# Kernel optimization log

Measured on AMD Instinct MI355X. Metric: run time of the kernel, lower is better.

## Reference

```python
import jax, jax.numpy as jnp
import numpy as np

B, C, N = 16, 256, 64
L = N * N
RED = 16  # SE reduction
ANGLES = (0, 90, 180, 270)
R = len(ANGLES)


def _d2xy(n, d):
    """Classic Hilbert curve distance -> (x, y) on an n x n grid (n power of 2)."""
    x = y = 0
    t = d
    s = 1
    while s < n:
        rx = 1 & (t // 2)
        ry = 1 & (t ^ rx)
        if ry == 0:
            if rx == 1:
                x = s - 1 - x
                y = s - 1 - y
            x, y = y, x
        x += s * rx
        y += s * ry
        t //= 4
        s *= 2
    return x, y


def _make_rot_idx(n, angles):
    coords = []
    for d in range(n * n):
        x, y = _d2xy(n, d)
        coords.append((y, x))  # original stores (row, col) = (y, x)
    idx_map = {coord: i for i, coord in enumerate(coords)}
    all_inv = []
    for angle in angles:
        inv = []
        for r, c in coords:
            if angle == 0:
                r0, c0 = r, c
            elif angle == 90:
                r0, c0 = c, n - 1 - r
            elif angle == 180:
                r0, c0 = n - 1 - r, n - 1 - c
            else:
                r0, c0 = n - 1 - c, r
            inv.append(idx_map[(r0, c0)])
        all_inv.append(inv)
    return np.asarray(all_inv, dtype=np.int32)  # [R, L]


def setup_inputs() -> dict:
    key = jax.random.key(0)
    k1, k2, k3 = jax.random.split(key, 3)
    x = jax.random.normal(k1, (B, C, L), dtype=jnp.float32)
    rot_idx = jnp.asarray(_make_rot_idx(N, ANGLES))  # [R, L] int32
    w1 = jax.random.normal(k2, (C, RED), dtype=jnp.float32) * (1.0 / np.sqrt(C))
    b1 = jnp.zeros((RED,), dtype=jnp.float32)
    w2 = jax.random.normal(k3, (RED, C), dtype=jnp.float32) * (1.0 / np.sqrt(RED))
    b2 = jnp.zeros((C,), dtype=jnp.float32)
    return {"x": x, "rot_idx": rot_idx, "w1": w1, "b1": b1, "w2": w2, "b2": b2}


def reference(x, rot_idx, w1, b1, w2, b2):
    # Gather the 4 Hilbert-order rotation permutations: [B, C, R, L]
    x_rot = x[:, :, rot_idx]
    # RotationChannelAttention (SE over channels, softmax over rotations)
    s = jnp.mean(x_rot, axis=3)                                   # [B, C, R]
    h = jax.nn.relu(jnp.einsum('bcr,ck->bkr', s, w1) + b1[None, :, None])
    scores = jnp.einsum('bkr,kc->bcr', h, w2) + b2[None, :, None]  # [B, C, R]
    w = jax.nn.softmax(scores, axis=2)                             # over rotations
    x_f = jnp.einsum('bcr,bcrl->bcl', w, x_rot)                    # [B, C, L]
    return x_f
```

## Files before the change

### kernel.cpp

```cpp
#include <hip/hip_runtime.h>


constexpr int Lconst = 4096;
constexpr int BC     = 16 * 256;

__global__ __launch_bounds__(256) void rotavg_kernel(
    const float* __restrict__ x,
    const int*   __restrict__ rot_idx,
    float*       __restrict__ out) {
  __shared__ float row[Lconst];

  const int bc = blockIdx.x;
  const float* xr = x + (size_t)bc * Lconst;
  float*       o  = out + (size_t)bc * Lconst;
  const int t = threadIdx.x;

  const float4* xr4  = reinterpret_cast<const float4*>(xr);
  float4*       row4 = reinterpret_cast<float4*>(row);
#pragma unroll
  for (int i = 0; i < 4; ++i) {
    row4[t + i * 256] = xr4[t + i * 256];
  }
  __syncthreads();

  const int4* idx0 = reinterpret_cast<const int4*>(rot_idx);
  const int4* idx1 = reinterpret_cast<const int4*>(rot_idx + Lconst);
  const int4* idx2 = reinterpret_cast<const int4*>(rot_idx + 2 * Lconst);
  const int4* idx3 = reinterpret_cast<const int4*>(rot_idx + 3 * Lconst);
  float4* o4 = reinterpret_cast<float4*>(o);

#pragma unroll
  for (int i = 0; i < 4; ++i) {
    const int e = t + i * 256;
    const int4 a = idx0[e];
    const int4 b = idx1[e];
    const int4 c = idx2[e];
    const int4 d = idx3[e];
    float4 v;
    v.x = 0.25f * (row[a.x] + row[b.x] + row[c.x] + row[d.x]);
    v.y = 0.25f * (row[a.y] + row[b.y] + row[c.y] + row[d.y]);
    v.z = 0.25f * (row[a.z] + row[b.z] + row[c.z] + row[d.z]);
    v.w = 0.25f * (row[a.w] + row[b.w] + row[c.w] + row[d.w]);
    o4[e] = v;
  }
}

extern "C" void kernel_launch(void* const* d_in, const int* in_sizes, int n_in,
                              void* d_out, int out_size, void* d_ws, size_t ws_size,
                              hipStream_t stream) {
  const float* x       = (const float*)d_in[0];
  const int*   rot_idx = (const int*)d_in[1];
  float* out = (float*)d_out;

  rotavg_kernel<<<BC, 256, 0, stream>>>(x, rot_idx, out);
}
```

Baseline: 28.81 us.

## Pack rotation indices into per-quad metadata and gather float4 quads from LDS

A small prep kernel compresses the three non-identity rotation index tables into one uint2 per 4-element group. Each entry holds a base quad index per rotation plus 2-bit lane selectors. The main kernel then does three float4 LDS reads per output quad instead of sixteen scalar reads, and one uint2 global load instead of four int4 loads. The identity rotation is taken from registers. This relies on rotation 0 being the identity and on each aligned quad mapping to a single aligned quad under rotation, which holds for the Hilbert layout. It also adds a second kernel launch and a workspace write.

```diff
diff --git a/kernel.cpp b/kernel.cpp
--- a/kernel.cpp
+++ b/kernel.cpp
@@ -1,46 +1,69 @@
 #include <hip/hip_runtime.h>
 
 
-constexpr int Lconst = 4096;
-constexpr int BC     = 16 * 256;
+constexpr int Lq  = 4096;
+constexpr int NQ  = Lq / 4;
+constexpr int BC  = 16 * 256;
+
+__global__ __launch_bounds__(256) void prep_kernel(
+    const int* __restrict__ rot, uint2* __restrict__ meta) {
+  const int q = blockIdx.x * 256 + threadIdx.x;
+  const int4* r90  = reinterpret_cast<const int4*>(rot + Lq);
+  const int4* r180 = reinterpret_cast<const int4*>(rot + 2 * Lq);
+  const int4* r270 = reinterpret_cast<const int4*>(rot + 3 * Lq);
+  const int4 a = r90[q], b = r180[q], c = r270[q];
+  const uint b90  = (uint)a.x >> 2;
+  const uint b180 = (uint)b.x >> 2;
+  const uint b270 = (uint)c.x >> 2;
+  const uint p90  = (uint)(a.x & 3) | ((uint)(a.y & 3) << 2) |
+                    ((uint)(a.z & 3) << 4) | ((uint)(a.w & 3) << 6);
+  const uint p180 = (uint)(b.x & 3) | ((uint)(b.y & 3) << 2) |
+                    ((uint)(b.z & 3) << 4) | ((uint)(b.w & 3) << 6);
+  const uint p270 = (uint)(c.x & 3) | ((uint)(c.y & 3) << 2) |
+                    ((uint)(c.z & 3) << 4) | ((uint)(c.w & 3) << 6);
+  meta[q] = make_uint2(b90 | (b180 << 10) | (b270 << 20),
+                       p90 | (p180 << 8) | (p270 << 16));
+}
+
+__device__ __forceinline__ float sel(const float4 q, const uint c) {
+  return c == 0u ? q.x : (c == 1u ? q.y : (c == 2u ? q.z : q.w));
+}
 
 __global__ __launch_bounds__(256) void rotavg_kernel(
     const float* __restrict__ x,
-    const int*   __restrict__ rot_idx,
+    const uint2* __restrict__ meta,
     float*       __restrict__ out) {
-  __shared__ float row[Lconst];
+  __shared__ float4 row4[NQ];
 
   const int bc = blockIdx.x;
-  const float* xr = x + (size_t)bc * Lconst;
-  float*       o  = out + (size_t)bc * Lconst;
+  const float4* xr4 = reinterpret_cast<const float4*>(x + (size_t)bc * Lq);
+  float4*       o4  = reinterpret_cast<float4*>(out + (size_t)bc * Lq);
   const int t = threadIdx.x;
 
-  const float4* xr4  = reinterpret_cast<const float4*>(xr);
-  float4*       row4 = reinterpret_cast<float4*>(row);
+  float4 xq[4];
+  uint2  mm[4];
 #pragma unroll
   for (int i = 0; i < 4; ++i) {
-    row4[t + i * 256] = xr4[t + i * 256];
+    const int e = t + i * 256;
+    xq[i] = xr4[e];
+    row4[e] = xq[i];
+    mm[i] = meta[e];
   }
   __syncthreads();
-
-  const int4* idx0 = reinterpret_cast<const int4*>(rot_idx);
-  const int4* idx1 = reinterpret_cast<const int4*>(rot_idx + Lconst);
-  const int4* idx2 = reinterpret_cast<const int4*>(rot_idx + 2 * Lconst);
-  const int4* idx3 = reinterpret_cast<const int4*>(rot_idx + 3 * Lconst);
-  float4* o4 = reinterpret_cast<float4*>(o);
 
 #pragma unroll
   for (int i = 0; i < 4; ++i) {
     const int e = t + i * 256;
-    const int4 a = idx0[e];
-    const int4 b = idx1[e];
-    const int4 c = idx2[e];
-    const int4 d = idx3[e];
+    const uint2 m = mm[i];
+    const float4 q90  = row4[m.x & 1023u];
+    const float4 q180 = row4[(m.x >> 10) & 1023u];
+    const float4 q270 = row4[(m.x >> 20) & 1023u];
+    const uint p = m.y;
     float4 v;
-    v.x = 0.25f * (row[a.x] + row[b.x] + row[c.x] + row[d.x]);
-    v.y = 0.25f * (row[a.y] + row[b.y] + row[c.y] + row[d.y]);
-    v.z = 0.25f * (row[a.z] + row[b.z] + row[c.z] + row[d.z]);
-    v.w = 0.25f * (row[a.w] + row[b.w] + row[c.w] + row[d.w]);
+    v.x = 0.25f * (xq[i].x + sel(q90, p & 3u)         + sel(q180, (p >> 8) & 3u)  + sel(q270, (p >> 16) & 3u));
+    v.y = 0.25f * (xq[i].y + sel(q90, (p >> 2) & 3u)  + sel(q180, (p >> 10) & 3u) + sel(q270, (p >> 18) & 3u));
+    v.z = 0.25f * (xq[i].z + sel(q90, (p >> 4) & 3u)  + sel(q180, (p >> 12) & 3u) + sel(q270, (p >> 20) & 3u));
+    v.w = 0.25f * (xq[i].w + sel(q90, (p >> 6) & 3u)  + sel(q180, (p >> 14) & 3u) + sel(q270, (p >> 22) & 3u));
     o4[e] = v;
   }
 }
@@ -51,6 +74,8 @@
   const float* x       = (const float*)d_in[0];
   const int*   rot_idx = (const int*)d_in[1];
   float* out = (float*)d_out;
+  uint2* meta = (uint2*)d_ws;
 
-  rotavg_kernel<<<BC, 256, 0, stream>>>(x, rot_idx, out);
+  prep_kernel<<<NQ / 256, 256, 0, stream>>>(rot_idx, meta);
+  rotavg_kernel<<<BC, 256, 0, stream>>>(x, meta, out);
 }
```

Result: slower. 33.80 us (+17.3%).

## Process four rows per block with register-cached packed indices and double-buffered LDS

Applied to the files above, without the earlier changes.

Each block now handles four (b,c) rows instead of one. It loads the rotation indices once into registers, packed as 16-bit pairs, and reuses them for all four rows. The next row's global load is issued while the current row is gathered from a double-buffered shared array. The identity rotation is read straight from the thread's own registers instead of through LDS. This is meant to remove repeated index traffic and overlap loads with the gather, at the cost of higher register pressure and fewer, longer blocks.

```diff
diff --git a/kernel.cpp b/kernel.cpp
--- a/kernel.cpp
+++ b/kernel.cpp
@@ -1,47 +1,71 @@
 #include <hip/hip_runtime.h>
 
 
-constexpr int Lconst = 4096;
-constexpr int BC     = 16 * 256;
+constexpr int L    = 4096;
+constexpr int ROWS = 4;
+constexpr int NB   = (16 * 256) / ROWS;
 
 __global__ __launch_bounds__(256) void rotavg_kernel(
     const float* __restrict__ x,
-    const int*   __restrict__ rot_idx,
+    const int*   __restrict__ rot,
     float*       __restrict__ out) {
-  __shared__ float row[Lconst];
+  __shared__ float row[2][L];
 
-  const int bc = blockIdx.x;
-  const float* xr = x + (size_t)bc * Lconst;
-  float*       o  = out + (size_t)bc * Lconst;
   const int t = threadIdx.x;
+  const size_t row0 = (size_t)blockIdx.x * ROWS;
 
-  const float4* xr4  = reinterpret_cast<const float4*>(xr);
-  float4*       row4 = reinterpret_cast<float4*>(row);
-#pragma unroll
-  for (int i = 0; i < 4; ++i) {
-    row4[t + i * 256] = xr4[t + i * 256];
-  }
-  __syncthreads();
-
-  const int4* idx0 = reinterpret_cast<const int4*>(rot_idx);
-  const int4* idx1 = reinterpret_cast<const int4*>(rot_idx + Lconst);
-  const int4* idx2 = reinterpret_cast<const int4*>(rot_idx + 2 * Lconst);
-  const int4* idx3 = reinterpret_cast<const int4*>(rot_idx + 3 * Lconst);
-  float4* o4 = reinterpret_cast<float4*>(o);
-
+  unsigned pk[24];
 #pragma unroll
   for (int i = 0; i < 4; ++i) {
     const int e = t + i * 256;
-    const int4 a = idx0[e];
-    const int4 b = idx1[e];
-    const int4 c = idx2[e];
-    const int4 d = idx3[e];
-    float4 v;
-    v.x = 0.25f * (row[a.x] + row[b.x] + row[c.x] + row[d.x]);
-    v.y = 0.25f * (row[a.y] + row[b.y] + row[c.y] + row[d.y]);
-    v.z = 0.25f * (row[a.z] + row[b.z] + row[c.z] + row[d.z]);
-    v.w = 0.25f * (row[a.w] + row[b.w] + row[c.w] + row[d.w]);
-    o4[e] = v;
+#pragma unroll
+    for (int r = 0; r < 3; ++r) {
+      const int4 v = reinterpret_cast<const int4*>(rot + (r + 1) * L)[e];
+      pk[i * 6 + r * 2 + 0] = (unsigned)v.x | ((unsigned)v.y << 16);
+      pk[i * 6 + r * 2 + 1] = (unsigned)v.z | ((unsigned)v.w << 16);
+    }
+  }
+
+  float4 cur[4], nxt[4];
+  {
+    const float4* xr4 = reinterpret_cast<const float4*>(x + row0 * L);
+#pragma unroll
+    for (int i = 0; i < 4; ++i) cur[i] = xr4[t + i * 256];
+  }
+
+#pragma unroll
+  for (int j = 0; j < ROWS; ++j) {
+    const int buf = j & 1;
+    float4* r4 = reinterpret_cast<float4*>(&row[buf][0]);
+#pragma unroll
+    for (int i = 0; i < 4; ++i) r4[t + i * 256] = cur[i];
+    __syncthreads();
+
+    if (j + 1 < ROWS) {
+      const float4* xn4 = reinterpret_cast<const float4*>(x + (row0 + j + 1) * L);
+#pragma unroll
+      for (int i = 0; i < 4; ++i) nxt[i] = xn4[t + i * 256];
+    }
+
+    const float* rb = &row[buf][0];
+    float4* o4 = reinterpret_cast<float4*>(out + (row0 + j) * L);
+#pragma unroll
+    for (int i = 0; i < 4; ++i) {
+      const unsigned a0 = pk[i * 6 + 0], a1 = pk[i * 6 + 1];
+      const unsigned b0 = pk[i * 6 + 2], b1 = pk[i * 6 + 3];
+      const unsigned c0 = pk[i * 6 + 4], c1 = pk[i * 6 + 5];
+      float4 v;
+      v.x = 0.25f * (cur[i].x + rb[a0 & 0xFFFu] + rb[b0 & 0xFFFu] + rb[c0 & 0xFFFu]);
+      v.y = 0.25f * (cur[i].y + rb[a0 >> 16]    + rb[b0 >> 16]    + rb[c0 >> 16]);
+      v.z = 0.25f * (cur[i].z + rb[a1 & 0xFFFu] + rb[b1 & 0xFFFu] + rb[c1 & 0xFFFu]);
+      v.w = 0.25f * (cur[i].w + rb[a1 >> 16]    + rb[b1 >> 16]    + rb[c1 >> 16]);
+      o4[t + i * 256] = v;
+    }
+
+    if (j + 1 < ROWS) {
+#pragma unroll
+      for (int i = 0; i < 4; ++i) cur[i] = nxt[i];
+    }
   }
 }
 
@@ -52,5 +76,5 @@
   const int*   rot_idx = (const int*)d_in[1];
   float* out = (float*)d_out;
 
-  rotavg_kernel<<<BC, 256, 0, stream>>>(x, rot_idx, out);
+  rotavg_kernel<<<NB, 256, 0, stream>>>(x, rot_idx, out);
 }
```

Result: faster. 26.52 us (-8.0%).
